# Kernel optimization log

Hardware: AMD Instinct MI355X
Metric: run time of the kernel (lower is better)

## Reference

```python
import jax, jax.numpy as jnp
import numpy as np

N_STEPS = 96
BATCH = 16384
N_MAT = 8
N_STRIKES = 8
PERIOD = 12          # N_steps // n_maturities
T_HORIZON = 1.0
RFR = 0.03
S0 = 1.0
LAYER = 128
DT = T_HORIZON / N_STEPS
SQRT_DT = float(np.sqrt(DT))
DF = float(np.exp(-RFR * DT))  # per-step discount factor


def _mlp(Win, bin_, Wh, bh, Wout, bout, x, out_fn):
    # x: [features, batch]; linear layers act on axis 0 (matches torch cat along dim 0)
    h = jax.nn.leaky_relu(Win @ x + bin_[:, None])
    for k in range(Wh.shape[0]):
        h = jax.nn.leaky_relu(Wh[k] @ h + bh[k][:, None])
    return out_fn(Wout @ h + bout[:, None])


def _forward(normals, strikes, lev_Win, lev_bin, lev_Wh, lev_bh, lev_Wout, lev_bout,
             hed_Win, hed_bin, hed_Wh, hed_bh, hed_Wout, hed_bout):
    B = normals.shape[1]
    dt = jnp.float32(DT)
    sqrt_dt = jnp.float32(SQRT_DT)
    r = jnp.float32(RFR)
    df = jnp.float32(DF)
    sg = jax.lax.stop_gradient

    def body(carry, xs):
        S_prev, hedging, prices, variance = carry
        i, nn_i = xs                      # i: int32 step (1..N_STEPS), nn_i: [B] normals
        i_f = i.astype(jnp.float32)
        idx = (i - 1) // PERIOD           # which per-period MLP
        t = ((i_f - 1.0) * dt) * jnp.ones((1, B), jnp.float32)
        X = jnp.concatenate([t, S_prev], axis=0)          # [2, B]
        lev = _mlp(lev_Win[idx], lev_bin[idx], lev_Wh[idx], lev_bh[idx],
                   lev_Wout[idx], lev_bout[idx], X, jax.nn.softplus)  # [1, B]
        drift = S_prev * r / (1.0 + jnp.abs(sg(S_prev) * r) * sqrt_dt)
        diffusion = S_prev * lev / (1.0 + jnp.abs(sg(S_prev * lev)) * sqrt_dt)
        dW = sqrt_dt * nn_i                               # [B]
        S_curr = S_prev + drift * dt + diffusion * dW     # [1, B]
        Xh = jnp.concatenate([t, sg(S_prev)], axis=0)
        hedge = _mlp(hed_Win[idx], hed_bin[idx], hed_Wh[idx], hed_bh[idx],
                     hed_Wout[idx], hed_bout[idx], Xh,
                     lambda y: y).reshape(N_STRIKES, N_MAT, B)
        hedging = hedging + (df ** (i_f - 1.0)) * sg(S_prev * diffusion) * hedge * dW
        # maturity handling (maturities at steps PERIOD, 2*PERIOD, ..., N_STEPS)
        table_idx = jnp.clip(i // PERIOD - 1, 0, N_MAT - 1)
        is_mat = (i % PERIOD == 0).astype(jnp.float32)
        simulated = (df ** i_f) * jnp.maximum(S_curr - strikes[:, None], 0.0) \
                    - hedging[:, table_idx]               # [K, B]
        mean = simulated.mean(axis=1)                     # [K]
        var = jnp.sum((simulated - mean[:, None]) ** 2, axis=1) / (B - 1)  # unbiased, as torch .var()
        prices = prices.at[:, table_idx].add(is_mat * mean)
        variance = variance.at[:, table_idx].add(is_mat * var)
        return (S_curr, hedging, prices, variance), None

    body = jax.checkpoint(body)
    carry0 = (jnp.full((1, B), jnp.float32(S0)),
              jnp.zeros((N_STRIKES, N_MAT, B), jnp.float32),
              jnp.zeros((N_STRIKES, N_MAT), jnp.float32),
              jnp.zeros((N_STRIKES, N_MAT), jnp.float32))
    xs = (jnp.arange(1, N_STEPS + 1, dtype=jnp.int32), normals)
    (_, _, prices, variance), _ = jax.lax.scan(body, carry0, xs)
    return prices, variance


def setup_inputs() -> dict:
    key = jax.random.key(0)
    ks = jax.random.split(key, 16)
    M, L, NH = N_MAT, LAYER, 3  # num_layers=4 -> 3 hidden-to-hidden layers

    def w(k, shape, fan_in):
        return (jax.random.normal(k, shape, jnp.float32) / np.sqrt(fan_in)).astype(jnp.float32)

    inp = {
        "normals": jax.random.normal(ks[0], (N_STEPS, BATCH), jnp.float32),
        "strikes": jnp.linspace(0.8, 1.15, N_STRIKES, dtype=jnp.float32),
        "lev_Win": w(ks[1], (M, L, 2), 2),
        "lev_bin": w(ks[2], (M, L), L),
        "lev_Wh": w(ks[3], (M, NH, L, L), L),
        "lev_bh": w(ks[4], (M, NH, L), L),
        "lev_Wout": w(ks[5], (M, 1, L), L),
        "lev_bout": w(ks[6], (M, 1), L),
        "hed_Win": w(ks[7], (M, L, 2), 2),
        "hed_bin": w(ks[8], (M, L), L),
        "hed_Wh": w(ks[9], (M, NH, L, L), L),
        "hed_bh": w(ks[10], (M, NH, L), L),
        "hed_Wout": w(ks[11], (M, N_STRIKES * N_MAT, L), L),
        "hed_bout": w(ks[12], (M, N_STRIKES * N_MAT), L),
    }
    return inp


def reference(normals, strikes, lev_Win, lev_bin, lev_Wh, lev_bh, lev_Wout, lev_bout,
              hed_Win, hed_bin, hed_Wh, hed_bh, hed_Wout, hed_bout):
    return _forward(normals, strikes, lev_Win, lev_bin, lev_Wh, lev_bh, lev_Wout, lev_bout,
                    hed_Win, hed_bin, hed_Wh, hed_bh, hed_Wout, hed_bout)
```

## Files before the change

### kernel.cpp

```cpp
#include <hip/hip_runtime.h>
#include <math.h>

typedef __attribute__((ext_vector_type(8)))  short  short8;
typedef __attribute__((ext_vector_type(4)))  short  short4v;
typedef __attribute__((ext_vector_type(16))) float  f32x16;
typedef __attribute__((ext_vector_type(4)))  float  f32x4v;

#define DT_F    ((float)(1.0/96.0))
#define SQDT_F  (0.10206207261596575f)
#define DF_F    (0.99968754882437816f)
#define RFR_F   (0.03f)

#define SWZ(c,k) (((c)<<7) + ((k) ^ (((c)&7)<<3)))

static __device__ __forceinline__ short f2bf(float x) {
    return __builtin_bit_cast(short, (__bf16)x);
}
static __device__ __forceinline__ float bf2f(short h) {
    return (float)__builtin_bit_cast(__bf16, h);
}

__device__ __forceinline__ void layer1(const float* __restrict__ Win, const float* __restrict__ bin_,
        float t, const float* __restrict__ sScur, ushort* __restrict__ out, int wvm, int l)
{
    const int g = l >> 4, c15 = l & 15;
    const int r0 = (wvm << 5) + (g << 3);
    float a8[8], w1[8];
#pragma unroll
    for (int jj = 0; jj < 8; ++jj) {
        const int r = r0 + jj;
        a8[jj] = fmaf(Win[2*r], t, bin_[r]);
        w1[jj] = Win[2*r + 1];
    }
#pragma unroll
    for (int cc = 0; cc < 4; ++cc) {
        const int c = c15 + (cc << 4);
        const float S = sScur[c];
        short8 v;
#pragma unroll
        for (int jj = 0; jj < 8; ++jj) {
            float h = fmaf(w1[jj], S, a8[jj]);
            h = fmaxf(h, 0.01f * h);
            v[jj] = f2bf(h);
        }
        *(short8*)&out[SWZ(c, r0)] = v;
    }
}

__device__ __forceinline__ void hidden32(const ushort* __restrict__ WFm, const float* __restrict__ bias,
        const ushort* __restrict__ bin, ushort* __restrict__ bout, int wvm, int l)
{
    const int c0 = l & 31;
    const int l5 = l >> 5;
    const int kr = l5 << 3;
    f32x16 a0e = {0,0,0,0,0,0,0,0,0,0,0,0,0,0,0,0};
    f32x16 a0o = a0e, a1e = a0e, a1o = a0e;
    const short8* fb = (const short8*)(WFm + (wvm << 12));
#pragma unroll
    for (int kc = 0; kc < 8; kc += 2) {
        short8 aE = fb[kc * 64 + l];
        short8 aO = fb[(kc + 1) * 64 + l];
        const int k0e = (kc << 4) + kr;
        const int k0o = k0e + 16;
        short8 b0e = *(const short8*)&bin[SWZ(c0,      k0e)];
        short8 b1e = *(const short8*)&bin[SWZ(c0 + 32, k0e)];
        short8 b0o = *(const short8*)&bin[SWZ(c0,      k0o)];
        short8 b1o = *(const short8*)&bin[SWZ(c0 + 32, k0o)];
        a0e = __builtin_amdgcn_mfma_f32_32x32x16_bf16(aE, b0e, a0e, 0, 0, 0);
        a1e = __builtin_amdgcn_mfma_f32_32x32x16_bf16(aE, b1e, a1e, 0, 0, 0);
        a0o = __builtin_amdgcn_mfma_f32_32x32x16_bf16(aO, b0o, a0o, 0, 0, 0);
        a1o = __builtin_amdgcn_mfma_f32_32x32x16_bf16(aO, b1o, a1o, 0, 0, 0);
    }
    const f32x16 acc0 = a0e + a0o;
    const f32x16 acc1 = a1e + a1o;
#pragma unroll
    for (int q = 0; q < 4; ++q) {
        const int rloc = (q << 3) + (l5 << 2);
        const f32x4v bq = *(const f32x4v*)&bias[(wvm << 5) + rloc];
        short4v o0, o1;
#pragma unroll
        for (int ii = 0; ii < 4; ++ii) {
            float x0 = acc0[(q << 2) + ii] + bq[ii]; o0[ii] = f2bf(fmaxf(x0, 0.01f * x0));
            float x1 = acc1[(q << 2) + ii] + bq[ii]; o1[ii] = f2bf(fmaxf(x1, 0.01f * x1));
        }
        *(short4v*)&bout[SWZ(c0,      (wvm << 5) + rloc)] = o0;
        *(short4v*)&bout[SWZ(c0 + 32, (wvm << 5) + rloc)] = o1;
    }
}

__global__ __launch_bounds__(512, 1)
void sim_kernel(const float* __restrict__ normals, const float* __restrict__ strikes,
                const float* __restrict__ levWin, const float* __restrict__ levbin,
                const float* __restrict__ levbh,  const float* __restrict__ levWout,
                const float* __restrict__ levbout,
                const float* __restrict__ hedWin, const float* __restrict__ hedbin,
                const float* __restrict__ hedbh,  const float* __restrict__ hedbout,
                const ushort* __restrict__ WF, double* __restrict__ accD)
{
    __shared__ ushort bufL[2][64 * 128];
    __shared__ ushort bufH[2][64 * 128];
    __shared__ float  sS[2][64];
    __shared__ float  sHc[64];

    const int tid  = threadIdx.x;
    const int wv   = tid >> 6;
    const int half = wv >> 2;
    const int wvm  = wv & 3;
    const int l    = tid & 63;
    const int g    = l >> 4;
    const int c15  = l & 15;
    const int bp0  = blockIdx.x * 64;

    if (tid < 64) sS[0][tid] = 1.0f;
    float hedg[4][4];
#pragma unroll
    for (int a = 0; a < 4; ++a)
#pragma unroll
        for (int b = 0; b < 4; ++b) hedg[a][b] = 0.f;
    float dfim1 = 1.0f;
    __syncthreads();

    for (int i = 1; i <= 96; ++i) {
        const int idx = (i - 1) / 12;
        const float t = (float)(i - 1) * DT_F;
        const float* sScur = sS[(i - 1) & 1];
        float* sSnxt = sS[i & 1];
        const ushort* WFi = WF + (size_t)idx * 106496;

        ushort* A = half ? bufH[0] : bufL[0];
        ushort* B = half ? bufH[1] : bufL[1];
        const float* Win  = (half ? hedWin : levWin) + idx * 256;
        const float* binp = (half ? hedbin : levbin) + (idx << 7);
        const float* bh   = (half ? hedbh  : levbh)  + idx * 384;
        const ushort* Wm  = WFi + ((half * 3) << 14);

        layer1(Win, binp, t, sScur, A, wvm, l);
        __syncthreads();
        hidden32(Wm,              bh,       A, B, wvm, l);
        __syncthreads();
        hidden32(Wm + 16384,      bh + 128, B, A, wvm, l);
        __syncthreads();
        hidden32(Wm + 32768,      bh + 256, A, B, wvm, l);
        __syncthreads();

        const float dfi = dfim1 * DF_F;
        f32x4v acc0 = {0,0,0,0}, acc1 = acc0, acc2 = acc0, acc3 = acc0;
        if (half == 0) {
            const float* Wo = levWout + (idx << 7);
            float wk[32];
#pragma unroll
            for (int kb = 0; kb < 8; ++kb)
                *(f32x4v*)&wk[4 * kb] = *(const f32x4v*)&Wo[(g << 5) + (kb << 2)];
            const int c = c15 + (wvm << 4);
            float p = 0.f;
#pragma unroll
            for (int kb = 0; kb < 4; ++kb) {
                short8 hv = *(const short8*)&bufL[1][SWZ(c, (g << 5) + (kb << 3))];
#pragma unroll
                for (int j = 0; j < 8; ++j) p = fmaf(bf2f(hv[j]), wk[(kb << 3) + j], p);
            }
            p += __shfl_xor(p, 16);
            p += __shfl_xor(p, 32);
            p += levbout[idx];
            const float lv = (p > 20.f) ? p : log1pf(expf(p));
            const float S = sScur[c];
            const float drift = S * RFR_F / (1.f + fabsf(S * RFR_F) * SQDT_F);
            const float dif   = S * lv    / (1.f + fabsf(S * lv)   * SQDT_F);
            const float dW = SQDT_F * normals[(i - 1) * 16384 + bp0 + c];
            const float Sn = S + drift * DT_F + dif * dW;
            if (g == 0) { sSnxt[c] = Sn; sHc[c] = dfim1 * (S * dif) * dW; }
        } else {
            const short8* fb = (const short8*)(WFi + 98304 + (wvm << 11));
            __builtin_amdgcn_s_setprio(1);
#pragma unroll
            for (int kcq = 0; kcq < 4; ++kcq) {
                short8 a = fb[kcq * 64 + l];
                const int k0 = (kcq << 5) + (g << 3);
                short8 b0 = *(const short8*)&bufH[1][SWZ(c15,      k0)];
                short8 b1 = *(const short8*)&bufH[1][SWZ(16 + c15, k0)];
                short8 b2 = *(const short8*)&bufH[1][SWZ(32 + c15, k0)];
                short8 b3 = *(const short8*)&bufH[1][SWZ(48 + c15, k0)];
                acc0 = __builtin_amdgcn_mfma_f32_16x16x32_bf16(a, b0, acc0, 0, 0, 0);
                acc1 = __builtin_amdgcn_mfma_f32_16x16x32_bf16(a, b1, acc1, 0, 0, 0);
                acc2 = __builtin_amdgcn_mfma_f32_16x16x32_bf16(a, b2, acc2, 0, 0, 0);
                acc3 = __builtin_amdgcn_mfma_f32_16x16x32_bf16(a, b3, acc3, 0, 0, 0);
            }
            __builtin_amdgcn_s_setprio(0);
        }
        __syncthreads();

        if (half == 1) {
            const f32x4v bo4 = *(const f32x4v*)&hedbout[(idx << 6) + (wvm << 4) + (g << 2)];
            const float hc0 = sHc[c15], hc1 = sHc[16 + c15], hc2 = sHc[32 + c15], hc3 = sHc[48 + c15];
#pragma unroll
            for (int ii = 0; ii < 4; ++ii) {
                hedg[0][ii] = fmaf(hc0, acc0[ii] + bo4[ii], hedg[0][ii]);
                hedg[1][ii] = fmaf(hc1, acc1[ii] + bo4[ii], hedg[1][ii]);
                hedg[2][ii] = fmaf(hc2, acc2[ii] + bo4[ii], hedg[2][ii]);
                hedg[3][ii] = fmaf(hc3, acc3[ii] + bo4[ii], hedg[3][ii]);
            }
            if ((i % 12) == 0) {
                const int m = i / 12 - 1;
                const int isel = m & 3;
                const bool active = ((m >> 2) == (g & 1));
                const int ks = (wvm << 1) + (g >> 1);
                float s_ = 0.f, q_ = 0.f;
                if (active) {
                    const float K = strikes[ks];
#pragma unroll
                    for (int ct = 0; ct < 4; ++ct) {
                        const float* hrow = hedg[ct];
                        const float hv = (isel == 0) ? hrow[0] : (isel == 1) ? hrow[1]
                                        : (isel == 2) ? hrow[2] : hrow[3];
                        const float Sn = sSnxt[(ct << 4) + c15];
                        const float sim = dfi * fmaxf(Sn - K, 0.f) - hv;
                        s_ += sim; q_ += sim * sim;
                    }
                }
#pragma unroll
                for (int off = 1; off < 16; off <<= 1) {
                    s_ += __shfl_xor(s_, off);
                    q_ += __shfl_xor(q_, off);
                }
                if (active && c15 == 0) {
                    const int rep = blockIdx.x & 31;
                    atomicAdd(&accD[rep * 128 + ks * 8 + m], (double)s_);
                    atomicAdd(&accD[rep * 128 + 64 + ks * 8 + m], (double)q_);
                }
            }
        }
        dfim1 = dfi;
    }
}

__global__ void prep_kernel(const float* __restrict__ levWh, const float* __restrict__ hedWh,
                            const float* __restrict__ hedWout,
                            ushort* __restrict__ WF, double* __restrict__ accD)
{
    const long long stride = (long long)gridDim.x * blockDim.x;
    const long long t0 = (long long)blockIdx.x * blockDim.x + threadIdx.x;
    for (long long e = t0; e < 851968LL; e += stride) {
        const int idx = (int)(e / 106496);
        const int rem = (int)(e % 106496);
        float val;
        if (rem < 98304) {
            const int m    = rem >> 14;
            const int r2   = rem & 16383;
            const int slot = r2 >> 9;
            const int rb   = slot >> 3;
            const int kc   = slot & 7;
            const int lane = (r2 >> 3) & 63;
            const int j    = r2 & 7;
            const int r = (rb << 5) + (lane & 31);
            const int k = (kc << 4) + ((lane >> 5) << 3) + j;
            const float* src = (m < 3) ? levWh : hedWh;
            const int mm = (m < 3) ? m : m - 3;
            val = src[(((idx * 3 + mm) << 7) + r) * 128 + k];
        } else {
            const int r3   = rem - 98304;
            const int slot = r3 >> 9;
            const int rb   = slot >> 2;
            const int kcq  = slot & 3;
            const int lane = (r3 >> 3) & 63;
            const int j    = r3 & 7;
            const int r = (rb << 4) + (lane & 15);
            const int k = (kcq << 5) + ((lane >> 4) << 3) + j;
            val = hedWout[(idx << 13) + (r << 7) + k];
        }
        WF[e] = (ushort)f2bf(val);
    }
    for (long long e = t0; e < 4096; e += stride) accD[e] = 0.0;
}

__global__ void finalize_kernel(const double* __restrict__ accD, float* __restrict__ out)
{
    const int t = threadIdx.x;
    if (t < 64) {
        double s = 0.0, q = 0.0;
        for (int rep = 0; rep < 32; ++rep) {
            s += accD[rep * 128 + t];
            q += accD[rep * 128 + 64 + t];
        }
        out[t]      = (float)(s / 16384.0);
        out[64 + t] = (float)((q - s * s / 16384.0) / 16383.0);
    }
}

extern "C" void kernel_launch(void* const* d_in, const int* in_sizes, int n_in,
                              void* d_out, int out_size, void* d_ws, size_t ws_size,
                              hipStream_t stream)
{
    const float* normals = (const float*)d_in[0];
    const float* strikes = (const float*)d_in[1];
    const float* levWin  = (const float*)d_in[2];
    const float* levbin  = (const float*)d_in[3];
    const float* levWh   = (const float*)d_in[4];
    const float* levbh   = (const float*)d_in[5];
    const float* levWout = (const float*)d_in[6];
    const float* levbout = (const float*)d_in[7];
    const float* hedWin  = (const float*)d_in[8];
    const float* hedbin  = (const float*)d_in[9];
    const float* hedWh   = (const float*)d_in[10];
    const float* hedbh   = (const float*)d_in[11];
    const float* hedWout = (const float*)d_in[12];
    const float* hedbout = (const float*)d_in[13];

    ushort* WF   = (ushort*)d_ws;
    double* accD = (double*)((char*)d_ws + 1703936);

    prep_kernel<<<1024, 256, 0, stream>>>(levWh, hedWh, hedWout, WF, accD);
    sim_kernel<<<256, 512, 0, stream>>>(normals, strikes,
                                        levWin, levbin, levbh, levWout, levbout,
                                        hedWin, hedbin, hedbh, hedbout,
                                        WF, accD);
    finalize_kernel<<<1, 64, 0, stream>>>(accD, (float*)d_out);
}
```

Baseline: 574.0 us.

## Cache per-period MLP weight fragments in registers and allow two blocks per CU

Hidden-layer and hedge-output MFMA weight fragments are loaded from global memory into registers once per 12-step period instead of every step, removing repeated global/L2 loads on the critical path of each layer. The hidden GEMM drops its even/odd split accumulators in favour of a single chain per output tile. Launch bounds are raised to two blocks per CU, which caps register use while the kernel now holds 28 extra short8 registers, risking spills. The single accumulator chain also lengthens MFMA dependency chains.

Measured after the change: 580.7 us. No clear change (+1.2%).

```diff
diff --git a/kernel.cpp b/kernel.cpp
--- a/kernel.cpp
+++ b/kernel.cpp
@@ -47,32 +47,22 @@
     }
 }
 
-__device__ __forceinline__ void hidden32(const ushort* __restrict__ WFm, const float* __restrict__ bias,
+__device__ __forceinline__ void hidden32(const short8 (&__restrict__ wf)[8], const float* __restrict__ bias,
         const ushort* __restrict__ bin, ushort* __restrict__ bout, int wvm, int l)
 {
     const int c0 = l & 31;
     const int l5 = l >> 5;
     const int kr = l5 << 3;
-    f32x16 a0e = {0,0,0,0,0,0,0,0,0,0,0,0,0,0,0,0};
-    f32x16 a0o = a0e, a1e = a0e, a1o = a0e;
-    const short8* fb = (const short8*)(WFm + (wvm << 12));
-#pragma unroll
-    for (int kc = 0; kc < 8; kc += 2) {
-        short8 aE = fb[kc * 64 + l];
-        short8 aO = fb[(kc + 1) * 64 + l];
-        const int k0e = (kc << 4) + kr;
-        const int k0o = k0e + 16;
-        short8 b0e = *(const short8*)&bin[SWZ(c0,      k0e)];
-        short8 b1e = *(const short8*)&bin[SWZ(c0 + 32, k0e)];
-        short8 b0o = *(const short8*)&bin[SWZ(c0,      k0o)];
-        short8 b1o = *(const short8*)&bin[SWZ(c0 + 32, k0o)];
-        a0e = __builtin_amdgcn_mfma_f32_32x32x16_bf16(aE, b0e, a0e, 0, 0, 0);
-        a1e = __builtin_amdgcn_mfma_f32_32x32x16_bf16(aE, b1e, a1e, 0, 0, 0);
-        a0o = __builtin_amdgcn_mfma_f32_32x32x16_bf16(aO, b0o, a0o, 0, 0, 0);
-        a1o = __builtin_amdgcn_mfma_f32_32x32x16_bf16(aO, b1o, a1o, 0, 0, 0);
-    }
-    const f32x16 acc0 = a0e + a0o;
-    const f32x16 acc1 = a1e + a1o;
+    f32x16 acc0 = {0,0,0,0,0,0,0,0,0,0,0,0,0,0,0,0};
+    f32x16 acc1 = acc0;
+#pragma unroll
+    for (int kc = 0; kc < 8; ++kc) {
+        const int k0 = (kc << 4) + kr;
+        short8 b0 = *(const short8*)&bin[SWZ(c0,      k0)];
+        short8 b1 = *(const short8*)&bin[SWZ(c0 + 32, k0)];
+        acc0 = __builtin_amdgcn_mfma_f32_32x32x16_bf16(wf[kc], b0, acc0, 0, 0, 0);
+        acc1 = __builtin_amdgcn_mfma_f32_32x32x16_bf16(wf[kc], b1, acc1, 0, 0, 0);
+    }
 #pragma unroll
     for (int q = 0; q < 4; ++q) {
         const int rloc = (q << 3) + (l5 << 2);
@@ -88,7 +78,7 @@
     }
 }
 
-__global__ __launch_bounds__(512, 1)
+__global__ __launch_bounds__(512, 2)
 void sim_kernel(const float* __restrict__ normals, const float* __restrict__ strikes,
                 const float* __restrict__ levWin, const float* __restrict__ levbin,
                 const float* __restrict__ levbh,  const float* __restrict__ levWout,
@@ -118,6 +108,9 @@
 #pragma unroll
         for (int b = 0; b < 4; ++b) hedg[a][b] = 0.f;
     float dfim1 = 1.0f;
+
+    short8 wCh[3][8];
+    short8 wOut[4];
     __syncthreads();
 
     for (int i = 1; i <= 96; ++i) {
@@ -127,20 +120,34 @@
         float* sSnxt = sS[i & 1];
         const ushort* WFi = WF + (size_t)idx * 106496;
 
+        if (((i - 1) % 12) == 0) {
+            const ushort* Wm = WFi + ((half * 3) << 14);
+#pragma unroll
+            for (int m = 0; m < 3; ++m) {
+                const short8* fb = (const short8*)(Wm + (m << 14) + (wvm << 12));
+#pragma unroll
+                for (int kc = 0; kc < 8; ++kc) wCh[m][kc] = fb[kc * 64 + l];
+            }
+            if (half) {
+                const short8* fo = (const short8*)(WFi + 98304 + (wvm << 11));
+#pragma unroll
+                for (int kcq = 0; kcq < 4; ++kcq) wOut[kcq] = fo[kcq * 64 + l];
+            }
+        }
+
         ushort* A = half ? bufH[0] : bufL[0];
         ushort* B = half ? bufH[1] : bufL[1];
         const float* Win  = (half ? hedWin : levWin) + idx * 256;
         const float* binp = (half ? hedbin : levbin) + (idx << 7);
         const float* bh   = (half ? hedbh  : levbh)  + idx * 384;
-        const ushort* Wm  = WFi + ((half * 3) << 14);
 
         layer1(Win, binp, t, sScur, A, wvm, l);
         __syncthreads();
-        hidden32(Wm,              bh,       A, B, wvm, l);
-        __syncthreads();
-        hidden32(Wm + 16384,      bh + 128, B, A, wvm, l);
-        __syncthreads();
-        hidden32(Wm + 32768,      bh + 256, A, B, wvm, l);
+        hidden32(wCh[0], bh,       A, B, wvm, l);
+        __syncthreads();
+        hidden32(wCh[1], bh + 128, B, A, wvm, l);
+        __syncthreads();
+        hidden32(wCh[2], bh + 256, A, B, wvm, l);
         __syncthreads();
 
         const float dfi = dfim1 * DF_F;
@@ -170,20 +177,18 @@
             const float Sn = S + drift * DT_F + dif * dW;
             if (g == 0) { sSnxt[c] = Sn; sHc[c] = dfim1 * (S * dif) * dW; }
         } else {
-            const short8* fb = (const short8*)(WFi + 98304 + (wvm << 11));
             __builtin_amdgcn_s_setprio(1);
 #pragma unroll
             for (int kcq = 0; kcq < 4; ++kcq) {
-                short8 a = fb[kcq * 64 + l];
                 const int k0 = (kcq << 5) + (g << 3);
                 short8 b0 = *(const short8*)&bufH[1][SWZ(c15,      k0)];
                 short8 b1 = *(const short8*)&bufH[1][SWZ(16 + c15, k0)];
                 short8 b2 = *(const short8*)&bufH[1][SWZ(32 + c15, k0)];
                 short8 b3 = *(const short8*)&bufH[1][SWZ(48 + c15, k0)];
-                acc0 = __builtin_amdgcn_mfma_f32_16x16x32_bf16(a, b0, acc0, 0, 0, 0);
-                acc1 = __builtin_amdgcn_mfma_f32_16x16x32_bf16(a, b1, acc1, 0, 0, 0);
-                acc2 = __builtin_amdgcn_mfma_f32_16x16x32_bf16(a, b2, acc2, 0, 0, 0);
-                acc3 = __builtin_amdgcn_mfma_f32_16x16x32_bf16(a, b3, acc3, 0, 0, 0);
+                acc0 = __builtin_amdgcn_mfma_f32_16x16x32_bf16(wOut[kcq], b0, acc0, 0, 0, 0);
+                acc1 = __builtin_amdgcn_mfma_f32_16x16x32_bf16(wOut[kcq], b1, acc1, 0, 0, 0);
+                acc2 = __builtin_amdgcn_mfma_f32_16x16x32_bf16(wOut[kcq], b2, acc2, 0, 0, 0);
+                acc3 = __builtin_amdgcn_mfma_f32_16x16x32_bf16(wOut[kcq], b3, acc3, 0, 0, 0);
             }
             __builtin_amdgcn_s_setprio(0);
         }
```

## Skew hedge MLP one stage behind leverage MLP to shorten per-step critical path

Applied to the files above, without the earlier changes.

The hedge half now runs its layers one phase behind the leverage half. Its output layer and the payoff accumulation are deferred into the next step's first phase and overlap with the leverage layer1, which removes one barrier-separated phase per time step. The change also raises launch bounds to allow two blocks per CU, swaps log1pf/expf for fast intrinsics in softplus, and prefetches the normal sample early. The risks are register pressure from the 2-block bound and slightly lower softplus accuracy.

Result: slower. 586.7 us (+2.2%).

```diff
diff --git a/kernel.cpp b/kernel.cpp
--- a/kernel.cpp
+++ b/kernel.cpp
@@ -88,7 +88,7 @@
     }
 }
 
-__global__ __launch_bounds__(512, 1)
+__global__ __launch_bounds__(512, 2)
 void sim_kernel(const float* __restrict__ normals, const float* __restrict__ strikes,
                 const float* __restrict__ levWin, const float* __restrict__ levbin,
                 const float* __restrict__ levbh,  const float* __restrict__ levWout,
@@ -118,7 +118,67 @@
 #pragma unroll
         for (int b = 0; b < 4; ++b) hedg[a][b] = 0.f;
     float dfim1 = 1.0f;
+    float nrm   = 0.f;
     __syncthreads();
+
+    auto hed_tail = [&](int j, float dfj) {
+        const int idxp = (j - 1) / 12;
+        const ushort* WFp = WF + (size_t)idxp * 106496;
+        f32x4v acc0 = {0,0,0,0}, acc1 = acc0, acc2 = acc0, acc3 = acc0;
+        const short8* fo = (const short8*)(WFp + 98304 + (wvm << 11));
+#pragma unroll
+        for (int kcq = 0; kcq < 4; ++kcq) {
+            short8 a = fo[kcq * 64 + l];
+            const int k0 = (kcq << 5) + (g << 3);
+            short8 b0 = *(const short8*)&bufH[1][SWZ(c15,      k0)];
+            short8 b1 = *(const short8*)&bufH[1][SWZ(16 + c15, k0)];
+            short8 b2 = *(const short8*)&bufH[1][SWZ(32 + c15, k0)];
+            short8 b3 = *(const short8*)&bufH[1][SWZ(48 + c15, k0)];
+            acc0 = __builtin_amdgcn_mfma_f32_16x16x32_bf16(a, b0, acc0, 0, 0, 0);
+            acc1 = __builtin_amdgcn_mfma_f32_16x16x32_bf16(a, b1, acc1, 0, 0, 0);
+            acc2 = __builtin_amdgcn_mfma_f32_16x16x32_bf16(a, b2, acc2, 0, 0, 0);
+            acc3 = __builtin_amdgcn_mfma_f32_16x16x32_bf16(a, b3, acc3, 0, 0, 0);
+        }
+        const f32x4v bo4 = *(const f32x4v*)&hedbout[(idxp << 6) + (wvm << 4) + (g << 2)];
+        const float hc0 = sHc[c15], hc1 = sHc[16 + c15], hc2 = sHc[32 + c15], hc3 = sHc[48 + c15];
+#pragma unroll
+        for (int ii = 0; ii < 4; ++ii) {
+            hedg[0][ii] = fmaf(hc0, acc0[ii] + bo4[ii], hedg[0][ii]);
+            hedg[1][ii] = fmaf(hc1, acc1[ii] + bo4[ii], hedg[1][ii]);
+            hedg[2][ii] = fmaf(hc2, acc2[ii] + bo4[ii], hedg[2][ii]);
+            hedg[3][ii] = fmaf(hc3, acc3[ii] + bo4[ii], hedg[3][ii]);
+        }
+        if ((j % 12) == 0) {
+            const int m = j / 12 - 1;
+            const int isel = m & 3;
+            const bool active = ((m >> 2) == (g & 1));
+            const int ks = (wvm << 1) + (g >> 1);
+            const float* sSj = sS[j & 1];
+            float s_ = 0.f, q_ = 0.f;
+            if (active) {
+                const float K = strikes[ks];
+#pragma unroll
+                for (int ct = 0; ct < 4; ++ct) {
+                    const float* hrow = hedg[ct];
+                    const float hv = (isel == 0) ? hrow[0] : (isel == 1) ? hrow[1]
+                                    : (isel == 2) ? hrow[2] : hrow[3];
+                    const float Sj = sSj[(ct << 4) + c15];
+                    const float sim = dfj * fmaxf(Sj - K, 0.f) - hv;
+                    s_ += sim; q_ += sim * sim;
+                }
+            }
+#pragma unroll
+            for (int off = 1; off < 16; off <<= 1) {
+                s_ += __shfl_xor(s_, off);
+                q_ += __shfl_xor(q_, off);
+            }
+            if (active && c15 == 0) {
+                const int rep = blockIdx.x & 31;
+                atomicAdd(&accD[rep * 128 + ks * 8 + m], (double)s_);
+                atomicAdd(&accD[rep * 128 + 64 + ks * 8 + m], (double)q_);
+            }
+        }
+    };
 
     for (int i = 1; i <= 96; ++i) {
         const int idx = (i - 1) / 12;
@@ -126,25 +186,29 @@
         const float* sScur = sS[(i - 1) & 1];
         float* sSnxt = sS[i & 1];
         const ushort* WFi = WF + (size_t)idx * 106496;
-
-        ushort* A = half ? bufH[0] : bufL[0];
-        ushort* B = half ? bufH[1] : bufL[1];
-        const float* Win  = (half ? hedWin : levWin) + idx * 256;
-        const float* binp = (half ? hedbin : levbin) + (idx << 7);
-        const float* bh   = (half ? hedbh  : levbh)  + idx * 384;
         const ushort* Wm  = WFi + ((half * 3) << 14);
-
-        layer1(Win, binp, t, sScur, A, wvm, l);
-        __syncthreads();
-        hidden32(Wm,              bh,       A, B, wvm, l);
-        __syncthreads();
-        hidden32(Wm + 16384,      bh + 128, B, A, wvm, l);
-        __syncthreads();
-        hidden32(Wm + 32768,      bh + 256, A, B, wvm, l);
-        __syncthreads();
-
-        const float dfi = dfim1 * DF_F;
-        f32x4v acc0 = {0,0,0,0}, acc1 = acc0, acc2 = acc0, acc3 = acc0;
+        const float* bh   = (half ? hedbh : levbh) + idx * 384;
+
+        if (half == 0) {
+            layer1(levWin + idx * 256, levbin + (idx << 7), t, sScur, bufL[0], wvm, l);
+            nrm = normals[(i - 1) * 16384 + bp0 + c15 + (wvm << 4)];
+        } else if (i > 1) {
+            hed_tail(i - 1, dfim1);
+        }
+        __syncthreads();
+
+        if (half == 0) hidden32(Wm,         bh,       bufL[0], bufL[1], wvm, l);
+        else           layer1(hedWin + idx * 256, hedbin + (idx << 7), t, sScur, bufH[0], wvm, l);
+        __syncthreads();
+
+        if (half == 0) hidden32(Wm + 16384, bh + 128, bufL[1], bufL[0], wvm, l);
+        else           hidden32(Wm,         bh,       bufH[0], bufH[1], wvm, l);
+        __syncthreads();
+
+        if (half == 0) hidden32(Wm + 32768, bh + 256, bufL[0], bufL[1], wvm, l);
+        else           hidden32(Wm + 16384, bh + 128, bufH[1], bufH[0], wvm, l);
+        __syncthreads();
+
         if (half == 0) {
             const float* Wo = levWout + (idx << 7);
             float wk[32];
@@ -162,75 +226,21 @@
             p += __shfl_xor(p, 16);
             p += __shfl_xor(p, 32);
             p += levbout[idx];
-            const float lv = (p > 20.f) ? p : log1pf(expf(p));
+            const float lv = (p > 20.f) ? p : __logf(1.f + __expf(p));
             const float S = sScur[c];
             const float drift = S * RFR_F / (1.f + fabsf(S * RFR_F) * SQDT_F);
             const float dif   = S * lv    / (1.f + fabsf(S * lv)   * SQDT_F);
-            const float dW = SQDT_F * normals[(i - 1) * 16384 + bp0 + c];
+            const float dW = SQDT_F * nrm;
             const float Sn = S + drift * DT_F + dif * dW;
             if (g == 0) { sSnxt[c] = Sn; sHc[c] = dfim1 * (S * dif) * dW; }
         } else {
-            const short8* fb = (const short8*)(WFi + 98304 + (wvm << 11));
-            __builtin_amdgcn_s_setprio(1);
-#pragma unroll
-            for (int kcq = 0; kcq < 4; ++kcq) {
-                short8 a = fb[kcq * 64 + l];
-                const int k0 = (kcq << 5) + (g << 3);
-                short8 b0 = *(const short8*)&bufH[1][SWZ(c15,      k0)];
-                short8 b1 = *(const short8*)&bufH[1][SWZ(16 + c15, k0)];
-                short8 b2 = *(const short8*)&bufH[1][SWZ(32 + c15, k0)];
-                short8 b3 = *(const short8*)&bufH[1][SWZ(48 + c15, k0)];
-                acc0 = __builtin_amdgcn_mfma_f32_16x16x32_bf16(a, b0, acc0, 0, 0, 0);
-                acc1 = __builtin_amdgcn_mfma_f32_16x16x32_bf16(a, b1, acc1, 0, 0, 0);
-                acc2 = __builtin_amdgcn_mfma_f32_16x16x32_bf16(a, b2, acc2, 0, 0, 0);
-                acc3 = __builtin_amdgcn_mfma_f32_16x16x32_bf16(a, b3, acc3, 0, 0, 0);
-            }
-            __builtin_amdgcn_s_setprio(0);
-        }
-        __syncthreads();
-
-        if (half == 1) {
-            const f32x4v bo4 = *(const f32x4v*)&hedbout[(idx << 6) + (wvm << 4) + (g << 2)];
-            const float hc0 = sHc[c15], hc1 = sHc[16 + c15], hc2 = sHc[32 + c15], hc3 = sHc[48 + c15];
-#pragma unroll
-            for (int ii = 0; ii < 4; ++ii) {
-                hedg[0][ii] = fmaf(hc0, acc0[ii] + bo4[ii], hedg[0][ii]);
-                hedg[1][ii] = fmaf(hc1, acc1[ii] + bo4[ii], hedg[1][ii]);
-                hedg[2][ii] = fmaf(hc2, acc2[ii] + bo4[ii], hedg[2][ii]);
-                hedg[3][ii] = fmaf(hc3, acc3[ii] + bo4[ii], hedg[3][ii]);
-            }
-            if ((i % 12) == 0) {
-                const int m = i / 12 - 1;
-                const int isel = m & 3;
-                const bool active = ((m >> 2) == (g & 1));
-                const int ks = (wvm << 1) + (g >> 1);
-                float s_ = 0.f, q_ = 0.f;
-                if (active) {
-                    const float K = strikes[ks];
-#pragma unroll
-                    for (int ct = 0; ct < 4; ++ct) {
-                        const float* hrow = hedg[ct];
-                        const float hv = (isel == 0) ? hrow[0] : (isel == 1) ? hrow[1]
-                                        : (isel == 2) ? hrow[2] : hrow[3];
-                        const float Sn = sSnxt[(ct << 4) + c15];
-                        const float sim = dfi * fmaxf(Sn - K, 0.f) - hv;
-                        s_ += sim; q_ += sim * sim;
-                    }
-                }
-#pragma unroll
-                for (int off = 1; off < 16; off <<= 1) {
-                    s_ += __shfl_xor(s_, off);
-                    q_ += __shfl_xor(q_, off);
-                }
-                if (active && c15 == 0) {
-                    const int rep = blockIdx.x & 31;
-                    atomicAdd(&accD[rep * 128 + ks * 8 + m], (double)s_);
-                    atomicAdd(&accD[rep * 128 + 64 + ks * 8 + m], (double)q_);
-                }
-            }
-        }
-        dfim1 = dfi;
-    }
+            hidden32(Wm + 32768, bh + 256, bufH[0], bufH[1], wvm, l);
+        }
+        dfim1 *= DF_F;
+        __syncthreads();
+    }
+
+    if (half == 1) hed_tail(96, dfim1);
 }
 
 __global__ void prep_kernel(const float* __restrict__ levWh, const float* __restrict__ hedWh,
```

## Halve per-block batch tile to 32 paths and launch twice as many blocks

Applied to the files above, without the earlier changes.

Each block now handles 32 Monte Carlo paths instead of 64, and the grid doubles to 512 blocks. Launch bounds allow up to four blocks per CU, so the work spreads over more CUs and more waves can overlap the many per-step barriers. The swizzle is widened to 16 rows. Smaller extras: the normal draw is loaded early, fast exp/log replace softplus's log1pf/expf, and the output bias is folded into the accumulator init. In exchange each MFMA weight fetch is reused over half as many columns, so more weight traffic per path, and the fast math may lose a little precision.

New measurement: 731.9 us. 1.27x slower.

```diff
diff --git a/kernel.cpp b/kernel.cpp
--- a/kernel.cpp
+++ b/kernel.cpp
@@ -11,7 +11,7 @@
 #define DF_F    (0.99968754882437816f)
 #define RFR_F   (0.03f)
 
-#define SWZ(c,k) (((c)<<7) + ((k) ^ (((c)&7)<<3)))
+#define SWZ(c,k) (((c)<<7) + ((k) ^ (((c)&15)<<3)))
 
 static __device__ __forceinline__ short f2bf(float x) {
     return __builtin_bit_cast(short, (__bf16)x);
@@ -33,7 +33,7 @@
         w1[jj] = Win[2*r + 1];
     }
 #pragma unroll
-    for (int cc = 0; cc < 4; ++cc) {
+    for (int cc = 0; cc < 2; ++cc) {
         const int c = c15 + (cc << 4);
         const float S = sScur[c];
         short8 v;
@@ -53,42 +53,35 @@
     const int c0 = l & 31;
     const int l5 = l >> 5;
     const int kr = l5 << 3;
-    f32x16 a0e = {0,0,0,0,0,0,0,0,0,0,0,0,0,0,0,0};
-    f32x16 a0o = a0e, a1e = a0e, a1o = a0e;
+    f32x16 ae = {0,0,0,0,0,0,0,0,0,0,0,0,0,0,0,0};
+    f32x16 ao = ae;
     const short8* fb = (const short8*)(WFm + (wvm << 12));
 #pragma unroll
     for (int kc = 0; kc < 8; kc += 2) {
         short8 aE = fb[kc * 64 + l];
         short8 aO = fb[(kc + 1) * 64 + l];
         const int k0e = (kc << 4) + kr;
-        const int k0o = k0e + 16;
-        short8 b0e = *(const short8*)&bin[SWZ(c0,      k0e)];
-        short8 b1e = *(const short8*)&bin[SWZ(c0 + 32, k0e)];
-        short8 b0o = *(const short8*)&bin[SWZ(c0,      k0o)];
-        short8 b1o = *(const short8*)&bin[SWZ(c0 + 32, k0o)];
-        a0e = __builtin_amdgcn_mfma_f32_32x32x16_bf16(aE, b0e, a0e, 0, 0, 0);
-        a1e = __builtin_amdgcn_mfma_f32_32x32x16_bf16(aE, b1e, a1e, 0, 0, 0);
-        a0o = __builtin_amdgcn_mfma_f32_32x32x16_bf16(aO, b0o, a0o, 0, 0, 0);
-        a1o = __builtin_amdgcn_mfma_f32_32x32x16_bf16(aO, b1o, a1o, 0, 0, 0);
-    }
-    const f32x16 acc0 = a0e + a0o;
-    const f32x16 acc1 = a1e + a1o;
+        short8 bE = *(const short8*)&bin[SWZ(c0, k0e)];
+        short8 bO = *(const short8*)&bin[SWZ(c0, k0e + 16)];
+        ae = __builtin_amdgcn_mfma_f32_32x32x16_bf16(aE, bE, ae, 0, 0, 0);
+        ao = __builtin_amdgcn_mfma_f32_32x32x16_bf16(aO, bO, ao, 0, 0, 0);
+    }
+    const f32x16 acc = ae + ao;
 #pragma unroll
     for (int q = 0; q < 4; ++q) {
         const int rloc = (q << 3) + (l5 << 2);
         const f32x4v bq = *(const f32x4v*)&bias[(wvm << 5) + rloc];
-        short4v o0, o1;
+        short4v o;
 #pragma unroll
         for (int ii = 0; ii < 4; ++ii) {
-            float x0 = acc0[(q << 2) + ii] + bq[ii]; o0[ii] = f2bf(fmaxf(x0, 0.01f * x0));
-            float x1 = acc1[(q << 2) + ii] + bq[ii]; o1[ii] = f2bf(fmaxf(x1, 0.01f * x1));
-        }
-        *(short4v*)&bout[SWZ(c0,      (wvm << 5) + rloc)] = o0;
-        *(short4v*)&bout[SWZ(c0 + 32, (wvm << 5) + rloc)] = o1;
-    }
-}
-
-__global__ __launch_bounds__(512, 1)
+            float x = acc[(q << 2) + ii] + bq[ii];
+            o[ii] = f2bf(fmaxf(x, 0.01f * x));
+        }
+        *(short4v*)&bout[SWZ(c0, (wvm << 5) + rloc)] = o;
+    }
+}
+
+__global__ __launch_bounds__(512, 4)
 void sim_kernel(const float* __restrict__ normals, const float* __restrict__ strikes,
                 const float* __restrict__ levWin, const float* __restrict__ levbin,
                 const float* __restrict__ levbh,  const float* __restrict__ levWout,
@@ -97,10 +90,10 @@
                 const float* __restrict__ hedbh,  const float* __restrict__ hedbout,
                 const ushort* __restrict__ WF, double* __restrict__ accD)
 {
-    __shared__ ushort bufL[2][64 * 128];
-    __shared__ ushort bufH[2][64 * 128];
-    __shared__ float  sS[2][64];
-    __shared__ float  sHc[64];
+    __shared__ ushort bufL[2][32 * 128];
+    __shared__ ushort bufH[2][32 * 128];
+    __shared__ float  sS[2][32];
+    __shared__ float  sHc[32];
 
     const int tid  = threadIdx.x;
     const int wv   = tid >> 6;
@@ -109,12 +102,12 @@
     const int l    = tid & 63;
     const int g    = l >> 4;
     const int c15  = l & 15;
-    const int bp0  = blockIdx.x * 64;
-
-    if (tid < 64) sS[0][tid] = 1.0f;
-    float hedg[4][4];
-#pragma unroll
-    for (int a = 0; a < 4; ++a)
+    const int bp0  = blockIdx.x * 32;
+
+    if (tid < 32) sS[0][tid] = 1.0f;
+    float hedg[2][4];
+#pragma unroll
+    for (int a = 0; a < 2; ++a)
 #pragma unroll
         for (int b = 0; b < 4; ++b) hedg[a][b] = 0.f;
     float dfim1 = 1.0f;
@@ -126,78 +119,76 @@
         const float* sScur = sS[(i - 1) & 1];
         float* sSnxt = sS[i & 1];
         const ushort* WFi = WF + (size_t)idx * 106496;
-
-        ushort* A = half ? bufH[0] : bufL[0];
-        ushort* B = half ? bufH[1] : bufL[1];
-        const float* Win  = (half ? hedWin : levWin) + idx * 256;
-        const float* binp = (half ? hedbin : levbin) + (idx << 7);
-        const float* bh   = (half ? hedbh  : levbh)  + idx * 384;
         const ushort* Wm  = WFi + ((half * 3) << 14);
-
-        layer1(Win, binp, t, sScur, A, wvm, l);
-        __syncthreads();
-        hidden32(Wm,              bh,       A, B, wvm, l);
-        __syncthreads();
-        hidden32(Wm + 16384,      bh + 128, B, A, wvm, l);
-        __syncthreads();
-        hidden32(Wm + 32768,      bh + 256, A, B, wvm, l);
+        const float* bh   = (half ? hedbh : levbh) + idx * 384;
+        ushort* buf0 = half ? bufH[0] : bufL[0];
+        ushort* buf1 = half ? bufH[1] : bufL[1];
+
+        layer1((half ? hedWin : levWin) + idx * 256,
+               (half ? hedbin : levbin) + (idx << 7), t, sScur, buf0, wvm, l);
+        float nrm = 0.f;
+        if (half == 0 && wvm < 2) nrm = normals[(i - 1) * 16384 + bp0 + c15 + (wvm << 4)];
+        __syncthreads();
+
+        hidden32(Wm,         bh,       buf0, buf1, wvm, l);
+        __syncthreads();
+        hidden32(Wm + 16384, bh + 128, buf1, buf0, wvm, l);
+        __syncthreads();
+        hidden32(Wm + 32768, bh + 256, buf0, buf1, wvm, l);
         __syncthreads();
 
         const float dfi = dfim1 * DF_F;
-        f32x4v acc0 = {0,0,0,0}, acc1 = acc0, acc2 = acc0, acc3 = acc0;
+        f32x4v acc0, acc1;
         if (half == 0) {
-            const float* Wo = levWout + (idx << 7);
-            float wk[32];
-#pragma unroll
-            for (int kb = 0; kb < 8; ++kb)
-                *(f32x4v*)&wk[4 * kb] = *(const f32x4v*)&Wo[(g << 5) + (kb << 2)];
-            const int c = c15 + (wvm << 4);
-            float p = 0.f;
-#pragma unroll
-            for (int kb = 0; kb < 4; ++kb) {
-                short8 hv = *(const short8*)&bufL[1][SWZ(c, (g << 5) + (kb << 3))];
-#pragma unroll
-                for (int j = 0; j < 8; ++j) p = fmaf(bf2f(hv[j]), wk[(kb << 3) + j], p);
+            if (wvm < 2) {
+                const float* Wo = levWout + (idx << 7);
+                float wk[32];
+#pragma unroll
+                for (int kb = 0; kb < 8; ++kb)
+                    *(f32x4v*)&wk[4 * kb] = *(const f32x4v*)&Wo[(g << 5) + (kb << 2)];
+                const int c = c15 + (wvm << 4);
+                float p = 0.f;
+#pragma unroll
+                for (int kb = 0; kb < 4; ++kb) {
+                    short8 hv = *(const short8*)&bufL[1][SWZ(c, (g << 5) + (kb << 3))];
+#pragma unroll
+                    for (int j = 0; j < 8; ++j) p = fmaf(bf2f(hv[j]), wk[(kb << 3) + j], p);
+                }
+                p += __shfl_xor(p, 16);
+                p += __shfl_xor(p, 32);
+                p += levbout[idx];
+                const float lv = (p > 20.f) ? p : __logf(1.f + __expf(p));
+                const float S = sScur[c];
+                const float drift = S * RFR_F / (1.f + fabsf(S * RFR_F) * SQDT_F);
+                const float dif   = S * lv    / (1.f + fabsf(S * lv)   * SQDT_F);
+                const float dW = SQDT_F * nrm;
+                const float Sn = S + drift * DT_F + dif * dW;
+                if (g == 0) { sSnxt[c] = Sn; sHc[c] = dfim1 * (S * dif) * dW; }
             }
-            p += __shfl_xor(p, 16);
-            p += __shfl_xor(p, 32);
-            p += levbout[idx];
-            const float lv = (p > 20.f) ? p : log1pf(expf(p));
-            const float S = sScur[c];
-            const float drift = S * RFR_F / (1.f + fabsf(S * RFR_F) * SQDT_F);
-            const float dif   = S * lv    / (1.f + fabsf(S * lv)   * SQDT_F);
-            const float dW = SQDT_F * normals[(i - 1) * 16384 + bp0 + c];
-            const float Sn = S + drift * DT_F + dif * dW;
-            if (g == 0) { sSnxt[c] = Sn; sHc[c] = dfim1 * (S * dif) * dW; }
         } else {
-            const short8* fb = (const short8*)(WFi + 98304 + (wvm << 11));
+            const short8* fo = (const short8*)(WFi + 98304 + (wvm << 11));
+            const f32x4v bo4 = *(const f32x4v*)&hedbout[(idx << 6) + (wvm << 4) + (g << 2)];
+            acc0 = bo4; acc1 = bo4;
             __builtin_amdgcn_s_setprio(1);
 #pragma unroll
             for (int kcq = 0; kcq < 4; ++kcq) {
-                short8 a = fb[kcq * 64 + l];
+                short8 a = fo[kcq * 64 + l];
                 const int k0 = (kcq << 5) + (g << 3);
                 short8 b0 = *(const short8*)&bufH[1][SWZ(c15,      k0)];
                 short8 b1 = *(const short8*)&bufH[1][SWZ(16 + c15, k0)];
-                short8 b2 = *(const short8*)&bufH[1][SWZ(32 + c15, k0)];
-                short8 b3 = *(const short8*)&bufH[1][SWZ(48 + c15, k0)];
                 acc0 = __builtin_amdgcn_mfma_f32_16x16x32_bf16(a, b0, acc0, 0, 0, 0);
                 acc1 = __builtin_amdgcn_mfma_f32_16x16x32_bf16(a, b1, acc1, 0, 0, 0);
-                acc2 = __builtin_amdgcn_mfma_f32_16x16x32_bf16(a, b2, acc2, 0, 0, 0);
-                acc3 = __builtin_amdgcn_mfma_f32_16x16x32_bf16(a, b3, acc3, 0, 0, 0);
             }
             __builtin_amdgcn_s_setprio(0);
         }
         __syncthreads();
 
         if (half == 1) {
-            const f32x4v bo4 = *(const f32x4v*)&hedbout[(idx << 6) + (wvm << 4) + (g << 2)];
-            const float hc0 = sHc[c15], hc1 = sHc[16 + c15], hc2 = sHc[32 + c15], hc3 = sHc[48 + c15];
+            const float hc0 = sHc[c15], hc1 = sHc[16 + c15];
 #pragma unroll
             for (int ii = 0; ii < 4; ++ii) {
-                hedg[0][ii] = fmaf(hc0, acc0[ii] + bo4[ii], hedg[0][ii]);
-                hedg[1][ii] = fmaf(hc1, acc1[ii] + bo4[ii], hedg[1][ii]);
-                hedg[2][ii] = fmaf(hc2, acc2[ii] + bo4[ii], hedg[2][ii]);
-                hedg[3][ii] = fmaf(hc3, acc3[ii] + bo4[ii], hedg[3][ii]);
+                hedg[0][ii] = fmaf(hc0, acc0[ii], hedg[0][ii]);
+                hedg[1][ii] = fmaf(hc1, acc1[ii], hedg[1][ii]);
             }
             if ((i % 12) == 0) {
                 const int m = i / 12 - 1;
@@ -208,7 +199,7 @@
                 if (active) {
                     const float K = strikes[ks];
 #pragma unroll
-                    for (int ct = 0; ct < 4; ++ct) {
+                    for (int ct = 0; ct < 2; ++ct) {
                         const float* hrow = hedg[ct];
                         const float hv = (isel == 0) ? hrow[0] : (isel == 1) ? hrow[1]
                                         : (isel == 2) ? hrow[2] : hrow[3];
@@ -309,7 +300,7 @@
     double* accD = (double*)((char*)d_ws + 1703936);
 
     prep_kernel<<<1024, 256, 0, stream>>>(levWh, hedWh, hedWout, WF, accD);
-    sim_kernel<<<256, 512, 0, stream>>>(normals, strikes,
+    sim_kernel<<<512, 512, 0, stream>>>(normals, strikes,
                                         levWin, levbin, levbh, levWout, levbout,
                                         hedWin, hedbin, hedbh, hedbout,
                                         WF, accD);
```
